# Optimization experiments

Hardware: AMD Instinct MI355X
Metric: run time of the kernel (lower is better)

## Reference

```python
import jax, jax.numpy as jnp
import numpy as np
import math

SUB = 0.8  # subset fraction (init kwarg)


def _capsule_weighted_average(x):
    # x: [B, I, O, D, H, W]; norm-weighted average over input caps (dim 1)
    n = jnp.linalg.norm(x, axis=3, keepdims=True)  # [B, I, O, 1, H, W]
    return (n * x).sum(axis=1) / n.sum(axis=1)      # [B, O, D, H, W]


def setup_inputs() -> dict:
    key = jax.random.key(0)
    # [B, input_caps, output_caps, pose_dim, H, W, kh, kw]
    x = jax.random.normal(key, (8, 32, 32, 8, 14, 14, 3, 3), dtype=jnp.float32)
    return {"x": x}


def reference(x):
    B, I, O, D, H, W = x.shape[:6]
    x = x.reshape(B, I, O, D, H, W, -1)             # flatten kernel positions -> K
    # norm-weighted average over the K kernel positions
    xn = jnp.linalg.norm(x, axis=3, keepdims=True)  # [B, I, O, 1, H, W, K]
    x = (xn * x).sum(axis=-1) / xn.sum(axis=-1)     # [B, I, O, D, H, W]

    v = _capsule_weighted_average(x)                # [B, O, D, H, W]

    # 'mse' metric: negative dot product between consensus v and each input capsule
    losses = -(v[:, None] * x).sum(axis=3)          # [B, I, O, H, W]
    subset_size = math.ceil(SUB * I)
    # kthvalue (k-th smallest) along input-caps dim
    thr = jnp.sort(losses, axis=1)[:, subset_size - 1:subset_size]  # [B, 1, O, H, W]
    choose = (losses <= thr).astype(x.dtype)[:, :, :, None]          # [B, I, O, 1, H, W]
    x = x * jax.lax.stop_gradient(choose)

    return _capsule_weighted_average(x)             # [B, O, D, H, W]
```

## Files before the change

kernel.cpp:

```cpp
#include <hip/hip_runtime.h>

#define B 8
#define I 32
#define O 32
#define D 8
#define H 14
#define W 14
#define K 9
#define WK (W*K)
#define DSTRIDE (H*W*K)
#define OSTRIDE (D*H*W*K)
#define ISTRIDE (O*D*H*W*K)
#define BSTRIDE ((size_t)I*ISTRIDE)
#define SUBSET 26
#define SLAB (D*H*WK)
#define SLAB4 (SLAB/4)
#define YS_BLOCK (I*W*D)

__global__ __launch_bounds__(256) void k_reduce(const float* __restrict__ x,
                                                float* __restrict__ ys) {
    const int bid = blockIdx.x;
    const int o = bid % O;
    const int i = (bid / O) % I;
    const int b = bid / (O * I);
    const int t = threadIdx.x;

    __shared__ float xs[SLAB];
    __shared__ float nk[DSTRIDE];

    const float4* src = (const float4*)(x + (size_t)b * BSTRIDE
                                          + (size_t)i * ISTRIDE
                                          + (size_t)o * OSTRIDE);
    float4* xs4 = (float4*)xs;
    #pragma unroll
    for (int it = 0; it < 14; ++it) {
        int idx = it * 256 + t;
        if (idx < SLAB4) xs4[idx] = src[idx];
    }
    __syncthreads();

    #pragma unroll
    for (int it = 0; it < 7; ++it) {
        int j = it * 256 + t;
        if (j < DSTRIDE) {
            float s = 0.f;
            #pragma unroll
            for (int d = 0; d < D; ++d) { float v = xs[d * DSTRIDE + j]; s += v * v; }
            nk[j] = sqrtf(s);
        }
    }
    __syncthreads();

    if (t < H * W) {
        const int h = t / W, w = t - (t / W) * W;
        const int jb = h * WK + w * K;
        float nkv[K];
        float den = 0.f;
        #pragma unroll
        for (int k = 0; k < K; ++k) { nkv[k] = nk[jb + k]; den += nkv[k]; }
        const float inv = 1.f / den;
        float y[D];
        #pragma unroll
        for (int d = 0; d < D; ++d) {
            float num = 0.f;
            #pragma unroll
            for (int k = 0; k < K; ++k) num += nkv[k] * xs[d * DSTRIDE + jb + k];
            y[d] = num * inv;
        }
        float4* dst = (float4*)(ys + ((((size_t)(b * O + o) * H + h) * I + i) * W + w) * D);
        dst[0] = make_float4(y[0], y[1], y[2], y[3]);
        dst[1] = make_float4(y[4], y[5], y[6], y[7]);
    }
}

__global__ __launch_bounds__(448) void k_route(const float* __restrict__ ys,
                                               float* __restrict__ out) {
    const int bid = blockIdx.x;
    const int h = bid % H;
    const int o = (bid / H) % O;
    const int b = bid / (H * O);
    const int t = threadIdx.x;
    const int i = t / W, w = t - (t / W) * W;

    __shared__ float ysl[YS_BLOCK];
    __shared__ float ns_s[I * W];
    __shared__ float ls_s[I * W];
    __shared__ float vsh[D * W];
    __shared__ float thr_s[W];

    const float4* src = (const float4*)(ys + (size_t)bid * YS_BLOCK);
    float4* ysl4 = (float4*)ysl;
    ysl4[t] = src[t];
    ysl4[t + 448] = src[t + 448];
    __syncthreads();

    float y[D];
    float s2 = 0.f;
    #pragma unroll
    for (int d = 0; d < D; ++d) { y[d] = ysl[t * D + d]; s2 += y[d] * y[d]; }
    const float nsv = sqrtf(s2);
    ns_s[t] = nsv;
    __syncthreads();

    if (t < D * W) {
        const int d = t / W, w2 = t - (t / W) * W;
        float num = 0.f, dn = 0.f;
        #pragma unroll
        for (int j = 0; j < I; ++j) {
            float nv = ns_s[j * W + w2];
            num += nv * ysl[(j * W + w2) * D + d];
            dn += nv;
        }
        vsh[d * W + w2] = num / dn;
    }
    __syncthreads();

    float lv = 0.f;
    #pragma unroll
    for (int d = 0; d < D; ++d) lv += vsh[d * W + w] * y[d];
    lv = -lv;
    ls_s[t] = lv;
    __syncthreads();

    int rank = 0;
    #pragma unroll
    for (int j = 0; j < I; ++j) {
        float lj = ls_s[j * W + w];
        rank += (lj < lv || (lj == lv && j < i)) ? 1 : 0;
    }
    if (rank == SUBSET - 1) thr_s[w] = lv;
    __syncthreads();

    if (t < D * W) {
        const int d = t / W, w2 = t - (t / W) * W;
        const float tw = thr_s[w2];
        float num = 0.f, dn = 0.f;
        #pragma unroll
        for (int j = 0; j < I; ++j) {
            float ls = ls_s[j * W + w2];
            float m  = (ls <= tw) ? 1.f : 0.f;
            float nv = m * ns_s[j * W + w2];
            num += nv * ysl[(j * W + w2) * D + d];
            dn  += nv;
        }
        out[(((size_t)b * O + o) * D + d) * (H * W) + h * W + w2] = num / dn;
    }
}

extern "C" void kernel_launch(void* const* d_in, const int* in_sizes, int n_in,
                              void* d_out, int out_size, void* d_ws, size_t ws_size,
                              hipStream_t stream) {
    const float* x = (const float*)d_in[0];
    float* out = (float*)d_out;
    float* ys = (float*)d_ws;

    k_reduce<<<dim3(B * I * O), dim3(256), 0, stream>>>(x, ys);
    k_route<<<dim3(B * O * H), dim3(448), 0, stream>>>(ys, out);
}
```

Baseline: 620.7 us.

## Pipeline k_reduce over row pairs with double-buffered shared memory and register prefetch

k_reduce no longer loads the whole 8x14x126 slab into LDS before computing. It now processes two h-rows at a time across seven iterations, prefetching the next chunk into registers with float2 loads while computing norms and weighted sums from a double-buffered LDS tile. The output is also computed one element per thread, spread over 224 threads, instead of one thread producing all 8 D values. This cuts LDS footprint, which should raise occupancy, and overlaps global loads with compute. The cost is more barriers per block and narrower float2 global loads.

```diff
diff --git a/kernel.cpp b/kernel.cpp
--- a/kernel.cpp
+++ b/kernel.cpp
@@ -13,8 +13,6 @@
 #define ISTRIDE (O*D*H*W*K)
 #define BSTRIDE ((size_t)I*ISTRIDE)
 #define SUBSET 26
-#define SLAB (D*H*WK)
-#define SLAB4 (SLAB/4)
 #define YS_BLOCK (I*W*D)
 
 __global__ __launch_bounds__(256) void k_reduce(const float* __restrict__ x,
@@ -25,51 +23,72 @@
     const int b = bid / (O * I);
     const int t = threadIdx.x;
 
-    __shared__ float xs[SLAB];
-    __shared__ float nk[DSTRIDE];
+    __shared__ float xs[2][D * 252];
+    __shared__ float nkl[2][256];
 
-    const float4* src = (const float4*)(x + (size_t)b * BSTRIDE
+    const float2* src = (const float2*)(x + (size_t)b * BSTRIDE
                                           + (size_t)i * ISTRIDE
                                           + (size_t)o * OSTRIDE);
-    float4* xs4 = (float4*)xs;
-    #pragma unroll
-    for (int it = 0; it < 14; ++it) {
-        int idx = it * 256 + t;
-        if (idx < SLAB4) xs4[idx] = src[idx];
-    }
-    __syncthreads();
+    const int f0 = t, f1 = t + 256, f2 = t + 512, f3 = t + 768;
+    const int d0 = f0 / 126, j0 = f0 - d0 * 126;
+    const int d1 = f1 / 126, j1 = f1 - d1 * 126;
+    const int d2 = f2 / 126, j2 = f2 - d2 * 126;
+    const int d3 = f3 / 126, j3 = f3 - d3 * 126;
+    const bool v3 = (f3 < 1008);
 
-    #pragma unroll
-    for (int it = 0; it < 7; ++it) {
-        int j = it * 256 + t;
-        if (j < DSTRIDE) {
+    const float2* p0 = src + d0 * 882 + j0;
+    const float2* p1 = src + d1 * 882 + j1;
+    const float2* p2 = src + d2 * 882 + j2;
+    const float2* p3 = src + d3 * 882 + j3;
+
+    float2 r0 = p0[0];
+    float2 r1 = p1[0];
+    float2 r2 = p2[0];
+    float2 r3 = v3 ? p3[0] : make_float2(0.f, 0.f);
+
+    float* ybase = ys + ((size_t)(b * O + o) * H * I + i) * (W * D);
+
+    const int row_y = t / 112;
+    const int rem_y = t - row_y * 112;
+    const int w_y = rem_y >> 3, d_y = rem_y & 7;
+
+    for (int rr = 0; rr < 7; ++rr) {
+        const int buf = rr & 1;
+        xs[buf][d0 * 252 + 2 * j0]     = r0.x;
+        xs[buf][d0 * 252 + 2 * j0 + 1] = r0.y;
+        xs[buf][d1 * 252 + 2 * j1]     = r1.x;
+        xs[buf][d1 * 252 + 2 * j1 + 1] = r1.y;
+        xs[buf][d2 * 252 + 2 * j2]     = r2.x;
+        xs[buf][d2 * 252 + 2 * j2 + 1] = r2.y;
+        if (v3) {
+            xs[buf][d3 * 252 + 2 * j3]     = r3.x;
+            xs[buf][d3 * 252 + 2 * j3 + 1] = r3.y;
+        }
+        __syncthreads();
+        if (rr + 1 < 7) {
+            r0 = p0[(rr + 1) * 126];
+            r1 = p1[(rr + 1) * 126];
+            r2 = p2[(rr + 1) * 126];
+            if (v3) r3 = p3[(rr + 1) * 126];
+        }
+        if (t < 252) {
             float s = 0.f;
             #pragma unroll
-            for (int d = 0; d < D; ++d) { float v = xs[d * DSTRIDE + j]; s += v * v; }
-            nk[j] = sqrtf(s);
+            for (int d = 0; d < D; ++d) { float v = xs[buf][d * 252 + t]; s += v * v; }
+            nkl[buf][t] = sqrtf(s);
         }
-    }
-    __syncthreads();
-
-    if (t < H * W) {
-        const int h = t / W, w = t - (t / W) * W;
-        const int jb = h * WK + w * K;
-        float nkv[K];
-        float den = 0.f;
-        #pragma unroll
-        for (int k = 0; k < K; ++k) { nkv[k] = nk[jb + k]; den += nkv[k]; }
-        const float inv = 1.f / den;
-        float y[D];
-        #pragma unroll
-        for (int d = 0; d < D; ++d) {
-            float num = 0.f;
+        __syncthreads();
+        if (t < 224) {
+            const int jb = row_y * 126 + w_y * K;
+            float den = 0.f, num = 0.f;
             #pragma unroll
-            for (int k = 0; k < K; ++k) num += nkv[k] * xs[d * DSTRIDE + jb + k];
-            y[d] = num * inv;
+            for (int k = 0; k < K; ++k) {
+                float nv = nkl[buf][jb + k];
+                den += nv;
+                num += nv * xs[buf][d_y * 252 + jb + k];
+            }
+            ybase[(size_t)(2 * rr + row_y) * (I * W * D) + rem_y] = num / den;
         }
-        float4* dst = (float4*)(ys + ((((size_t)(b * O + o) * H + h) * I + i) * W + w) * D);
-        dst[0] = make_float4(y[0], y[1], y[2], y[3]);
-        dst[1] = make_float4(y[4], y[5], y[6], y[7]);
     }
 }
 
```

Result: no change. 616.9 us (-0.6%).
